# Optimization experiments

Hardware: AMD Instinct MI355X
Metric: run time of the kernel (lower is better)

Reference implementation:

```python
import jax, jax.numpy as jnp
import numpy as np

B, X, Y, Z = 8, 32, 32, 32
Dx = Dy = Dz = 128
K = 256   # h_dim * k, k=1
H = 2     # h_out
EPS = 1e-5


def _wn(V, g):
    # weight_norm with dim=None: W = g * V / ||V||_F (g scalar)
    return (g / jnp.linalg.norm(V)) * V


def setup_inputs() -> dict:
    key = jax.random.key(0)
    ks = jax.random.split(key, 8)
    x = jax.random.normal(ks[0], (B, X, Dx), jnp.float32)
    y = jax.random.normal(ks[1], (B, Y, Dy), jnp.float32)
    z = jax.random.normal(ks[2], (B, Z, Dz), jnp.float32)
    Vx = jax.random.normal(ks[3], (K, Dx), jnp.float32) * 0.05
    Vy = jax.random.normal(ks[4], (K, Dy), jnp.float32) * 0.05
    Vz = jax.random.normal(ks[5], (K, Dz), jnp.float32) * 0.05
    Vh = jax.random.normal(ks[6], (H, K), jnp.float32) * 0.05
    return {
        "x": x, "y": y, "z": z,
        "Vx": Vx, "gx": jnp.linalg.norm(Vx), "bx": jnp.zeros((K,), jnp.float32),
        "Vy": Vy, "gy": jnp.linalg.norm(Vy), "by": jnp.zeros((K,), jnp.float32),
        "Vz": Vz, "gz": jnp.linalg.norm(Vz), "bz": jnp.zeros((K,), jnp.float32),
        "Vh": Vh, "gh": jnp.linalg.norm(Vh), "bh": jnp.zeros((H,), jnp.float32),
        "gamma": jnp.ones((K,), jnp.float32), "beta": jnp.zeros((K,), jnp.float32),
    }


def reference(x, y, z, Vx, gx, bx, Vy, gy, by, Vz, gz, bz, Vh, gh, bh, gamma, beta):
    relu = jax.nn.relu
    _x = relu(x @ _wn(Vx, gx).T + bx)  # [B,X,K]
    _y = relu(y @ _wn(Vy, gy).T + by)  # [B,Y,K]
    _z = relu(z @ _wn(Vz, gz).T + bz)  # [B,Z,K]
    # trilinear outer product: [B,X,Y,Z,K] (memory-explosive intermediate)
    xyz = jnp.einsum('bxk,byk,bzk->bxyzk', _x, _y, _z)
    att = jnp.einsum('bxyzk,hk->bhxyz', xyz, _wn(Vh, gh)) + bh[None, :, None, None, None]
    # softmax over flattened X*Y*Z per head
    att = jax.nn.softmax(att.reshape(B, H, -1), axis=-1).reshape(B, H, X, Y, Z)
    # attention pooling, summed over all h_out heads (equals the torch loop)
    att_sum = att.sum(axis=1)  # [B,X,Y,Z]
    logits = jnp.einsum('bxk,byk,bzk,bxyz->bk', _x, _y, _z, att_sum)  # [B,K]
    # BatchNorm1d (training-mode batch stats, biased variance)
    mean = logits.mean(axis=0)
    var = logits.var(axis=0)
    out = (logits - mean) / jnp.sqrt(var + EPS) * gamma + beta
    return (out, att)
```

## Files before the change

### kernel.cpp

```cpp
#include <hip/hip_runtime.h>
#include <math.h>

#define BB 8
#define XD 32
#define DD 128
#define KK 256
#define HH 2
#define XYZ 32768
#define EPSV 1e-5f

#define WS_X    0
#define WS_Y    65536
#define WS_Z    131072
#define WS_RAW  196608
#define WS_SM   (WS_RAW + 524288)
#define WS_LOG  (WS_SM + 1024)

__global__ void __launch_bounds__(256)
tan_proj_kernel(const float* x, const float* y, const float* z,
                const float* Vx, const float* Vy, const float* Vz,
                const float* gx, const float* gy, const float* gz,
                const float* bx, const float* by, const float* bz,
                float* ws) {
    __shared__ float lin[4 * DD];
    __shared__ float wred[4];
    int bid = blockIdx.x;
    int which = bid >> 6;
    int rgrp = bid & 63;
    int r0 = rgrp * 4;
    const float *in, *V, *g, *bias;
    float* outp;
    if (which == 0)      { in = x; V = Vx; g = gx; bias = bx; outp = ws + WS_X; }
    else if (which == 1) { in = y; V = Vy; g = gy; bias = by; outp = ws + WS_Y; }
    else                 { in = z; V = Vz; g = gz; bias = bz; outp = ws + WS_Z; }
    int t = threadIdx.x;
    {
        int f0 = t, f1 = t + 256;
        lin[f0] = in[(r0 + (f0 >> 7)) * DD + (f0 & 127)];
        lin[f1] = in[(r0 + (f1 >> 7)) * DD + (f1 & 127)];
    }
    __syncthreads();
    const float4* v4 = (const float4*)(V + t * DD);
    const float4* l4 = (const float4*)lin;
    float a0 = 0.f, a1 = 0.f, a2 = 0.f, a3 = 0.f, ssp = 0.f;
#pragma unroll 8
    for (int d4 = 0; d4 < DD / 4; ++d4) {
        float4 a = v4[d4];
        ssp += a.x * a.x + a.y * a.y + a.z * a.z + a.w * a.w;
        float4 b0 = l4[d4];
        float4 b1 = l4[32 + d4];
        float4 b2 = l4[64 + d4];
        float4 b3 = l4[96 + d4];
        a0 += a.x * b0.x + a.y * b0.y + a.z * b0.z + a.w * b0.w;
        a1 += a.x * b1.x + a.y * b1.y + a.z * b1.z + a.w * b1.w;
        a2 += a.x * b2.x + a.y * b2.y + a.z * b2.z + a.w * b2.w;
        a3 += a.x * b3.x + a.y * b3.y + a.z * b3.z + a.w * b3.w;
    }
#pragma unroll
    for (int o = 32; o > 0; o >>= 1) ssp += __shfl_xor(ssp, o);
    if ((t & 63) == 0) wred[t >> 6] = ssp;
    __syncthreads();
    float ss = wred[0] + wred[1] + wred[2] + wred[3];
    float scale = g[0] * rsqrtf(ss);
    float bv = bias[t];
    outp[(r0 + 0) * KK + t] = fmaxf(a0 * scale + bv, 0.f);
    outp[(r0 + 1) * KK + t] = fmaxf(a1 * scale + bv, 0.f);
    outp[(r0 + 2) * KK + t] = fmaxf(a2 * scale + bv, 0.f);
    outp[(r0 + 3) * KK + t] = fmaxf(a3 * scale + bv, 0.f);
}

__global__ void __launch_bounds__(256)
tan_score_kernel(const float* Vh, const float* gh, const float* bh, float* ws) {
    __shared__ float ys[32 * 256];
    __shared__ float zs[32 * 256];
    __shared__ float shh;
    __shared__ float smred[4][4];
    int t = threadIdx.x;
    int bb = blockIdx.x >> 5;
    int xx = blockIdx.x & 31;
    const float* _xb = ws + WS_X + (bb * 32 + xx) * KK;
    const float* _yb = ws + WS_Y + bb * 8192;
    const float* _zb = ws + WS_Z + bb * 8192;

    if (t < 64) {
        float4 h1 = *(const float4*)(Vh + t * 8);
        float4 h2 = *(const float4*)(Vh + t * 8 + 4);
        float hs = h1.x * h1.x + h1.y * h1.y + h1.z * h1.z + h1.w * h1.w
                 + h2.x * h2.x + h2.y * h2.y + h2.z * h2.z + h2.w * h2.w;
#pragma unroll
        for (int o = 32; o > 0; o >>= 1) hs += __shfl_xor(hs, o);
        if (t == 0) shh = hs;
    }

#pragma unroll
    for (int i = 0; i < 8; ++i) {
        int flat = i * 1024 + t * 4;
        int row = flat >> 8;
        int k = flat & 255;
        int gsw = (((k >> 2) ^ (row & 7)) << 2);
        *(float4*)(ys + row * 256 + gsw) = *(const float4*)(_yb + flat);
        *(float4*)(zs + row * 256 + gsw) = *(const float4*)(_zb + flat);
    }
    __syncthreads();
    float sh = gh[0] * rsqrtf(shh);

    int ty = t >> 4;
    int tz = t & 15;
    int y0 = ty, y1 = ty + 16;
    int z0 = tz, z1 = tz + 15 + 1;
    int ysw0 = (y0 & 7), ysw1 = (y1 & 7);
    int zsw0 = (z0 & 7), zsw1 = (z1 & 7);

    float a000 = 0.f, a001 = 0.f, a010 = 0.f, a011 = 0.f;
    float a100 = 0.f, a101 = 0.f, a110 = 0.f, a111 = 0.f;

#pragma unroll 4
    for (int kc = 0; kc < 256; kc += 4) {
        int g = kc >> 2;
        float4 xv  = *(const float4*)(_xb + kc);
        float4 vh0 = *(const float4*)(Vh + kc);
        float4 vh1 = *(const float4*)(Vh + KK + kc);
        float4 ya = *(const float4*)(ys + y0 * 256 + ((g ^ ysw0) << 2));
        float4 yb = *(const float4*)(ys + y1 * 256 + ((g ^ ysw1) << 2));
        float4 za = *(const float4*)(zs + z0 * 256 + ((g ^ zsw0) << 2));
        float4 zb = *(const float4*)(zs + z1 * 256 + ((g ^ zsw1) << 2));
#define TAN_STEP(c) { \
        float xs = sh * xv.c; \
        float w0 = xs * vh0.c, w1 = xs * vh1.c; \
        float t00 = w0 * ya.c, t01 = w0 * yb.c; \
        float t10 = w1 * ya.c, t11 = w1 * yb.c; \
        a000 = fmaf(t00, za.c, a000); a001 = fmaf(t00, zb.c, a001); \
        a010 = fmaf(t01, za.c, a010); a011 = fmaf(t01, zb.c, a011); \
        a100 = fmaf(t10, za.c, a100); a101 = fmaf(t10, zb.c, a101); \
        a110 = fmaf(t11, za.c, a110); a111 = fmaf(t11, zb.c, a111); }
        TAN_STEP(x) TAN_STEP(y) TAN_STEP(z) TAN_STEP(w)
#undef TAN_STEP
    }

    float b0 = bh[0], b1 = bh[1];
    a000 += b0; a001 += b0; a010 += b0; a011 += b0;
    a100 += b1; a101 += b1; a110 += b1; a111 += b1;
    float* r0 = ws + WS_RAW + (bb * 2 + 0) * XYZ + xx * 1024;
    float* r1 = r0 + XYZ;
    r0[y0 * 32 + z0] = a000;  r0[y0 * 32 + z1] = a001;
    r0[y1 * 32 + z0] = a010;  r0[y1 * 32 + z1] = a011;
    r1[y0 * 32 + z0] = a100;  r1[y0 * 32 + z1] = a101;
    r1[y1 * 32 + z0] = a110;  r1[y1 * 32 + z1] = a111;

    float m0 = fmaxf(fmaxf(a000, a001), fmaxf(a010, a011));
    float l0 = __expf(a000 - m0) + __expf(a001 - m0)
             + __expf(a010 - m0) + __expf(a011 - m0);
    float m1 = fmaxf(fmaxf(a100, a101), fmaxf(a110, a111));
    float l1 = __expf(a100 - m1) + __expf(a101 - m1)
             + __expf(a110 - m1) + __expf(a111 - m1);
#pragma unroll
    for (int o = 1; o < 64; o <<= 1) {
        float mo = __shfl_xor(m0, o), lo = __shfl_xor(l0, o);
        float nm = fmaxf(m0, mo);
        l0 = l0 * __expf(m0 - nm) + lo * __expf(mo - nm); m0 = nm;
        mo = __shfl_xor(m1, o); lo = __shfl_xor(l1, o);
        nm = fmaxf(m1, mo);
        l1 = l1 * __expf(m1 - nm) + lo * __expf(mo - nm); m1 = nm;
    }
    if ((t & 63) == 0) {
        int w = t >> 6;
        smred[w][0] = m0; smred[w][1] = l0;
        smred[w][2] = m1; smred[w][3] = l1;
    }
    __syncthreads();
    if (t == 0) {
        float M0 = smred[0][0], L0 = smred[0][1];
        float M1 = smred[0][2], L1 = smred[0][3];
#pragma unroll
        for (int w = 1; w < 4; ++w) {
            float nm = fmaxf(M0, smred[w][0]);
            L0 = L0 * __expf(M0 - nm) + smred[w][1] * __expf(smred[w][0] - nm);
            M0 = nm;
            nm = fmaxf(M1, smred[w][2]);
            L1 = L1 * __expf(M1 - nm) + smred[w][3] * __expf(smred[w][2] - nm);
            M1 = nm;
        }
        float* sm = ws + WS_SM + (bb * 32 + xx) * 4;
        sm[0] = M0; sm[1] = L0; sm[2] = M1; sm[3] = L1;
    }
}

__global__ void __launch_bounds__(256)
tan_logits_kernel(float* ws, float* out) {
    __shared__ float as4[1024];
    __shared__ float cons[4];
    int b = blockIdx.x >> 5;
    int x = blockIdx.x & 31;
    int t = threadIdx.x;
    const float* _zb = ws + WS_Z + b * 8192;
    float zreg[32];
#pragma unroll
    for (int zi = 0; zi < 32; ++zi) zreg[zi] = _zb[zi * 256 + t];

    if (t < 64) {
        const float* sm = ws + WS_SM + (b * 32 + (t & 31)) * 4;
        float4 p = *(const float4*)sm;
        float m0 = p.x, l0 = p.y, m1 = p.z, l1 = p.w;
#pragma unroll
        for (int o = 1; o < 32; o <<= 1) {
            float mo = __shfl_xor(m0, o), lo = __shfl_xor(l0, o);
            float nm = fmaxf(m0, mo);
            l0 = l0 * __expf(m0 - nm) + lo * __expf(mo - nm); m0 = nm;
            mo = __shfl_xor(m1, o); lo = __shfl_xor(l1, o);
            nm = fmaxf(m1, mo);
            l1 = l1 * __expf(m1 - nm) + lo * __expf(mo - nm); m1 = nm;
        }
        if (t == 0) {
            cons[0] = m0; cons[1] = 1.f / l0;
            cons[2] = m1; cons[3] = 1.f / l1;
        }
    }
    __syncthreads();
    float M0 = cons[0], inv0 = cons[1], M1 = cons[2], inv1 = cons[3];
    const float* r0 = ws + WS_RAW + (b * 2) * XYZ + x * 1024;
    const float* r1 = r0 + XYZ;
    float* o0 = out + BB * KK + (b * 2) * XYZ + x * 1024;
    float* o1 = o0 + XYZ;
#pragma unroll
    for (int i = t; i < 1024; i += 256) {
        float a0 = __expf(r0[i] - M0) * inv0;
        float a1 = __expf(r1[i] - M1) * inv1;
        o0[i] = a0; o1[i] = a1;
        as4[i] = a0 + a1;
    }
    __syncthreads();

    const float* _yb = ws + WS_Y + b * 8192;
    float acc = 0.f;
#pragma unroll 4
    for (int y = 0; y < 32; ++y) {
        float s = 0.f;
        const float4* ar = (const float4*)(as4 + y * 32);
#pragma unroll
        for (int j = 0; j < 8; ++j) {
            float4 a = ar[j];
            s += a.x * zreg[j * 4] + a.y * zreg[j * 4 + 1]
               + a.z * zreg[j * 4 + 2] + a.w * zreg[j * 4 + 3];
        }
        acc = fmaf(_yb[y * 256 + t], s, acc);
    }
    float xv = ws[WS_X + (b * 32 + x) * 256 + t];
    atomicAdd(ws + WS_LOG + b * 256 + t, xv * acc);
}

__global__ void __launch_bounds__(256)
tan_bn_kernel(const float* ws, const float* gamma, const float* beta, float* out) {
    int k = threadIdx.x;
    const float* lgp = ws + WS_LOG;
    float lg[BB];
#pragma unroll
    for (int b = 0; b < BB; ++b) lg[b] = lgp[b * 256 + k];
    float mean = 0.f;
#pragma unroll
    for (int b = 0; b < BB; ++b) mean += lg[b];
    mean *= 0.125f;
    float var = 0.f;
#pragma unroll
    for (int b = 0; b < BB; ++b) { float d = lg[b] - mean; var += d * d; }
    var *= 0.125f;
    float inv = rsqrtf(var + EPSV);
    float gm = gamma[k], bt = beta[k];
#pragma unroll
    for (int b = 0; b < BB; ++b)
        out[b * 256 + k] = (lg[b] - mean) * inv * gm + bt;
}

extern "C" void kernel_launch(void* const* d_in, const int* in_sizes, int n_in,
                              void* d_out, int out_size, void* d_ws, size_t ws_size,
                              hipStream_t stream) {
    (void)in_sizes; (void)n_in; (void)out_size; (void)ws_size;
    const float* x     = (const float*)d_in[0];
    const float* y     = (const float*)d_in[1];
    const float* z     = (const float*)d_in[2];
    const float* Vx    = (const float*)d_in[3];
    const float* gx    = (const float*)d_in[4];
    const float* bx    = (const float*)d_in[5];
    const float* Vy    = (const float*)d_in[6];
    const float* gy    = (const float*)d_in[7];
    const float* by    = (const float*)d_in[8];
    const float* Vz    = (const float*)d_in[9];
    const float* gz    = (const float*)d_in[10];
    const float* bz    = (const float*)d_in[11];
    const float* Vh    = (const float*)d_in[12];
    const float* gh    = (const float*)d_in[13];
    const float* bh    = (const float*)d_in[14];
    const float* gamma = (const float*)d_in[15];
    const float* beta  = (const float*)d_in[16];
    float* ws  = (float*)d_ws;
    float* out = (float*)d_out;

    hipMemsetAsync(ws + WS_LOG, 0, 2048 * sizeof(float), stream);
    tan_proj_kernel<<<192, 256, 0, stream>>>(x, y, z, Vx, Vy, Vz,
                                             gx, gy, gz, bx, by, bz, ws);
    tan_score_kernel<<<256, 256, 0, stream>>>(Vh, gh, bh, ws);
    tan_logits_kernel<<<256, 256, 0, stream>>>(ws, out);
    tan_bn_kernel<<<1, 256, 0, stream>>>(ws, gamma, beta, out);
}
```

Measured before the change: 121.7 us.

## Fuse all stages into one cooperative kernel with grid syncs, keep scores on-chip

Replaces the memset and four kernel launches with a single cooperative kernel that separates projection, scoring, softmax/pooling and batchnorm with grid-wide syncs. The raw attention scores stay in registers across the softmax-statistics sync, so the 2 MB workspace round trip is gone. Y/Z values are read from shared memory instead of global, and attention output is written with coalesced float4 stores. The trade-off is grid.sync cost and a requirement that all 256 blocks be co-resident; the 64 KB of shared memory per block may limit occupancy.

```diff
diff --git a/kernel.cpp b/kernel.cpp
--- a/kernel.cpp
+++ b/kernel.cpp
@@ -1,96 +1,103 @@
 #include <hip/hip_runtime.h>
+#include <hip/hip_cooperative_groups.h>
 #include <math.h>
 
+namespace cg = cooperative_groups;
+
 #define BB 8
-#define XD 32
 #define DD 128
 #define KK 256
-#define HH 2
 #define XYZ 32768
 #define EPSV 1e-5f
 
 #define WS_X    0
 #define WS_Y    65536
 #define WS_Z    131072
-#define WS_RAW  196608
-#define WS_SM   (WS_RAW + 524288)
-#define WS_LOG  (WS_SM + 1024)
+#define WS_SM   196608
+#define WS_SHH  (WS_SM + 1024)
+#define WS_LOG  (WS_SHH + 16)
 
 __global__ void __launch_bounds__(256)
-tan_proj_kernel(const float* x, const float* y, const float* z,
-                const float* Vx, const float* Vy, const float* Vz,
-                const float* gx, const float* gy, const float* gz,
-                const float* bx, const float* by, const float* bz,
-                float* ws) {
+tan_fused_kernel(const float* x, const float* y, const float* z,
+                 const float* Vx, const float* Vy, const float* Vz,
+                 const float* gx, const float* gy, const float* gz,
+                 const float* bx, const float* by, const float* bz,
+                 const float* Vh, const float* gh, const float* bh,
+                 const float* gamma, const float* beta,
+                 float* ws, float* out) {
+    cg::grid_group grid = cg::this_grid();
+    __shared__ float smem[16384];
     __shared__ float lin[4 * DD];
     __shared__ float wred[4];
+    __shared__ float smred[4][4];
+    __shared__ float cons[4];
+
+    int t = threadIdx.x;
     int bid = blockIdx.x;
-    int which = bid >> 6;
-    int rgrp = bid & 63;
-    int r0 = rgrp * 4;
-    const float *in, *V, *g, *bias;
-    float* outp;
-    if (which == 0)      { in = x; V = Vx; g = gx; bias = bx; outp = ws + WS_X; }
-    else if (which == 1) { in = y; V = Vy; g = gy; bias = by; outp = ws + WS_Y; }
-    else                 { in = z; V = Vz; g = gz; bias = bz; outp = ws + WS_Z; }
-    int t = threadIdx.x;
-    {
+
+    if (bid < 192) {
+        int which = bid >> 6;
+        int r0 = (bid & 63) * 4;
+        const float *in, *V, *g, *bias;
+        float* outp;
+        if (which == 0)      { in = x; V = Vx; g = gx; bias = bx; outp = ws + WS_X; }
+        else if (which == 1) { in = y; V = Vy; g = gy; bias = by; outp = ws + WS_Y; }
+        else                 { in = z; V = Vz; g = gz; bias = bz; outp = ws + WS_Z; }
         int f0 = t, f1 = t + 256;
         lin[f0] = in[(r0 + (f0 >> 7)) * DD + (f0 & 127)];
         lin[f1] = in[(r0 + (f1 >> 7)) * DD + (f1 & 127)];
-    }
-    __syncthreads();
-    const float4* v4 = (const float4*)(V + t * DD);
-    const float4* l4 = (const float4*)lin;
-    float a0 = 0.f, a1 = 0.f, a2 = 0.f, a3 = 0.f, ssp = 0.f;
+        __syncthreads();
+        const float4* v4 = (const float4*)(V + t * DD);
+        const float4* l4 = (const float4*)lin;
+        float a0 = 0.f, a1 = 0.f, a2 = 0.f, a3 = 0.f, ssp = 0.f;
 #pragma unroll 8
-    for (int d4 = 0; d4 < DD / 4; ++d4) {
-        float4 a = v4[d4];
-        ssp += a.x * a.x + a.y * a.y + a.z * a.z + a.w * a.w;
-        float4 b0 = l4[d4];
-        float4 b1 = l4[32 + d4];
-        float4 b2 = l4[64 + d4];
-        float4 b3 = l4[96 + d4];
-        a0 += a.x * b0.x + a.y * b0.y + a.z * b0.z + a.w * b0.w;
-        a1 += a.x * b1.x + a.y * b1.y + a.z * b1.z + a.w * b1.w;
-        a2 += a.x * b2.x + a.y * b2.y + a.z * b2.z + a.w * b2.w;
-        a3 += a.x * b3.x + a.y * b3.y + a.z * b3.z + a.w * b3.w;
-    }
-#pragma unroll
-    for (int o = 32; o > 0; o >>= 1) ssp += __shfl_xor(ssp, o);
-    if ((t & 63) == 0) wred[t >> 6] = ssp;
-    __syncthreads();
-    float ss = wred[0] + wred[1] + wred[2] + wred[3];
-    float scale = g[0] * rsqrtf(ss);
-    float bv = bias[t];
-    outp[(r0 + 0) * KK + t] = fmaxf(a0 * scale + bv, 0.f);
-    outp[(r0 + 1) * KK + t] = fmaxf(a1 * scale + bv, 0.f);
-    outp[(r0 + 2) * KK + t] = fmaxf(a2 * scale + bv, 0.f);
-    outp[(r0 + 3) * KK + t] = fmaxf(a3 * scale + bv, 0.f);
-}
-
-__global__ void __launch_bounds__(256)
-tan_score_kernel(const float* Vh, const float* gh, const float* bh, float* ws) {
-    __shared__ float ys[32 * 256];
-    __shared__ float zs[32 * 256];
-    __shared__ float shh;
-    __shared__ float smred[4][4];
-    int t = threadIdx.x;
-    int bb = blockIdx.x >> 5;
-    int xx = blockIdx.x & 31;
+        for (int d4 = 0; d4 < DD / 4; ++d4) {
+            float4 a = v4[d4];
+            ssp += a.x * a.x + a.y * a.y + a.z * a.z + a.w * a.w;
+            float4 b0 = l4[d4];
+            float4 b1 = l4[32 + d4];
+            float4 b2 = l4[64 + d4];
+            float4 b3 = l4[96 + d4];
+            a0 += a.x * b0.x + a.y * b0.y + a.z * b0.z + a.w * b0.w;
+            a1 += a.x * b1.x + a.y * b1.y + a.z * b1.z + a.w * b1.w;
+            a2 += a.x * b2.x + a.y * b2.y + a.z * b2.z + a.w * b2.w;
+            a3 += a.x * b3.x + a.y * b3.y + a.z * b3.z + a.w * b3.w;
+        }
+#pragma unroll
+        for (int o = 32; o > 0; o >>= 1) ssp += __shfl_xor(ssp, o);
+        if ((t & 63) == 0) wred[t >> 6] = ssp;
+        __syncthreads();
+        float ss = wred[0] + wred[1] + wred[2] + wred[3];
+        float scale = g[0] * rsqrtf(ss);
+        float bv = bias[t];
+        outp[(r0 + 0) * KK + t] = fmaxf(a0 * scale + bv, 0.f);
+        outp[(r0 + 1) * KK + t] = fmaxf(a1 * scale + bv, 0.f);
+        outp[(r0 + 2) * KK + t] = fmaxf(a2 * scale + bv, 0.f);
+        outp[(r0 + 3) * KK + t] = fmaxf(a3 * scale + bv, 0.f);
+    } else if (bid == 192) {
+        for (int i = t; i < 2048; i += 256) ws[WS_LOG + i] = 0.f;
+    } else if (bid == 193) {
+        if (t < 64) {
+            float4 h1 = *(const float4*)(Vh + t * 8);
+            float4 h2 = *(const float4*)(Vh + t * 8 + 4);
+            float hs = h1.x * h1.x + h1.y * h1.y + h1.z * h1.z + h1.w * h1.w
+                     + h2.x * h2.x + h2.y * h2.y + h2.z * h2.z + h2.w * h2.w;
+#pragma unroll
+            for (int o = 32; o > 0; o >>= 1) hs += __shfl_xor(hs, o);
+            if (t == 0) ws[WS_SHH] = hs;
+        }
+    }
+    __threadfence();
+    grid.sync();
+
+    int bb = bid >> 5;
+    int xx = bid & 31;
     const float* _xb = ws + WS_X + (bb * 32 + xx) * KK;
     const float* _yb = ws + WS_Y + bb * 8192;
     const float* _zb = ws + WS_Z + bb * 8192;
-
-    if (t < 64) {
-        float4 h1 = *(const float4*)(Vh + t * 8);
-        float4 h2 = *(const float4*)(Vh + t * 8 + 4);
-        float hs = h1.x * h1.x + h1.y * h1.y + h1.z * h1.z + h1.w * h1.w
-                 + h2.x * h2.x + h2.y * h2.y + h2.z * h2.z + h2.w * h2.w;
-#pragma unroll
-        for (int o = 32; o > 0; o >>= 1) hs += __shfl_xor(hs, o);
-        if (t == 0) shh = hs;
-    }
+    float sh = gh[0] * rsqrtf(ws[WS_SHH]);
+    float* ys = smem;
+    float* zs = smem + 8192;
 
 #pragma unroll
     for (int i = 0; i < 8; ++i) {
@@ -102,12 +109,11 @@
         *(float4*)(zs + row * 256 + gsw) = *(const float4*)(_zb + flat);
     }
     __syncthreads();
-    float sh = gh[0] * rsqrtf(shh);
 
     int ty = t >> 4;
     int tz = t & 15;
     int y0 = ty, y1 = ty + 16;
-    int z0 = tz, z1 = tz + 15 + 1;
+    int z0 = tz, z1 = tz + 16;
     int ysw0 = (y0 & 7), ysw1 = (y1 & 7);
     int zsw0 = (z0 & 7), zsw1 = (z1 & 7);
 
@@ -140,12 +146,14 @@
     float b0 = bh[0], b1 = bh[1];
     a000 += b0; a001 += b0; a010 += b0; a011 += b0;
     a100 += b1; a101 += b1; a110 += b1; a111 += b1;
-    float* r0 = ws + WS_RAW + (bb * 2 + 0) * XYZ + xx * 1024;
-    float* r1 = r0 + XYZ;
-    r0[y0 * 32 + z0] = a000;  r0[y0 * 32 + z1] = a001;
-    r0[y1 * 32 + z0] = a010;  r0[y1 * 32 + z1] = a011;
-    r1[y0 * 32 + z0] = a100;  r1[y0 * 32 + z1] = a101;
-    r1[y1 * 32 + z0] = a110;  r1[y1 * 32 + z1] = a111;
+
+    float yreg[32], zreg[32];
+#pragma unroll
+    for (int r = 0; r < 32; ++r) {
+        int sw = ((((t >> 2) ^ (r & 7)) << 2) | (t & 3));
+        yreg[r] = ys[r * 256 + sw];
+        zreg[r] = zs[r * 256 + sw];
+    }
 
     float m0 = fmaxf(fmaxf(a000, a001), fmaxf(a010, a011));
     float l0 = __expf(a000 - m0) + __expf(a001 - m0)
@@ -183,91 +191,92 @@
         float* sm = ws + WS_SM + (bb * 32 + xx) * 4;
         sm[0] = M0; sm[1] = L0; sm[2] = M1; sm[3] = L1;
     }
-}
-
-__global__ void __launch_bounds__(256)
-tan_logits_kernel(float* ws, float* out) {
-    __shared__ float as4[1024];
-    __shared__ float cons[4];
-    int b = blockIdx.x >> 5;
-    int x = blockIdx.x & 31;
-    int t = threadIdx.x;
-    const float* _zb = ws + WS_Z + b * 8192;
-    float zreg[32];
-#pragma unroll
-    for (int zi = 0; zi < 32; ++zi) zreg[zi] = _zb[zi * 256 + t];
+    __threadfence();
+    grid.sync();
 
     if (t < 64) {
-        const float* sm = ws + WS_SM + (b * 32 + (t & 31)) * 4;
+        const float* sm = ws + WS_SM + (bb * 32 + (t & 31)) * 4;
         float4 p = *(const float4*)sm;
-        float m0 = p.x, l0 = p.y, m1 = p.z, l1 = p.w;
+        float fm0 = p.x, fl0 = p.y, fm1 = p.z, fl1 = p.w;
 #pragma unroll
         for (int o = 1; o < 32; o <<= 1) {
-            float mo = __shfl_xor(m0, o), lo = __shfl_xor(l0, o);
-            float nm = fmaxf(m0, mo);
-            l0 = l0 * __expf(m0 - nm) + lo * __expf(mo - nm); m0 = nm;
-            mo = __shfl_xor(m1, o); lo = __shfl_xor(l1, o);
-            nm = fmaxf(m1, mo);
-            l1 = l1 * __expf(m1 - nm) + lo * __expf(mo - nm); m1 = nm;
+            float mo = __shfl_xor(fm0, o), lo = __shfl_xor(fl0, o);
+            float nm = fmaxf(fm0, mo);
+            fl0 = fl0 * __expf(fm0 - nm) + lo * __expf(mo - nm); fm0 = nm;
+            mo = __shfl_xor(fm1, o); lo = __shfl_xor(fl1, o);
+            nm = fmaxf(fm1, mo);
+            fl1 = fl1 * __expf(fm1 - nm) + lo * __expf(mo - nm); fm1 = nm;
         }
         if (t == 0) {
-            cons[0] = m0; cons[1] = 1.f / l0;
-            cons[2] = m1; cons[3] = 1.f / l1;
+            cons[0] = fm0; cons[1] = 1.f / fl0;
+            cons[2] = fm1; cons[3] = 1.f / fl1;
         }
     }
     __syncthreads();
     float M0 = cons[0], inv0 = cons[1], M1 = cons[2], inv1 = cons[3];
-    const float* r0 = ws + WS_RAW + (b * 2) * XYZ + x * 1024;
-    const float* r1 = r0 + XYZ;
-    float* o0 = out + BB * KK + (b * 2) * XYZ + x * 1024;
-    float* o1 = o0 + XYZ;
-#pragma unroll
-    for (int i = t; i < 1024; i += 256) {
-        float a0 = __expf(r0[i] - M0) * inv0;
-        float a1 = __expf(r1[i] - M1) * inv1;
-        o0[i] = a0; o1[i] = a1;
-        as4[i] = a0 + a1;
-    }
+
+    float* e0p = smem;
+    float* e1p = smem + 1024;
+    float* as4 = smem + 2048;
+    float e000 = __expf(a000 - M0) * inv0;
+    float e001 = __expf(a001 - M0) * inv0;
+    float e010 = __expf(a010 - M0) * inv0;
+    float e011 = __expf(a011 - M0) * inv0;
+    float e100 = __expf(a100 - M1) * inv1;
+    float e101 = __expf(a101 - M1) * inv1;
+    float e110 = __expf(a110 - M1) * inv1;
+    float e111 = __expf(a111 - M1) * inv1;
+    e0p[y0 * 32 + z0] = e000;  e0p[y0 * 32 + z1] = e001;
+    e0p[y1 * 32 + z0] = e010;  e0p[y1 * 32 + z1] = e011;
+    e1p[y0 * 32 + z0] = e100;  e1p[y0 * 32 + z1] = e101;
+    e1p[y1 * 32 + z0] = e110;  e1p[y1 * 32 + z1] = e111;
+    as4[y0 * 32 + z0] = e000 + e100;  as4[y0 * 32 + z1] = e001 + e101;
+    as4[y1 * 32 + z0] = e010 + e110;  as4[y1 * 32 + z1] = e011 + e111;
     __syncthreads();
 
-    const float* _yb = ws + WS_Y + b * 8192;
+    float4* o0 = (float4*)(out + BB * KK + (bb * 2) * XYZ + xx * 1024);
+    float4* o1 = o0 + XYZ / 4;
+    o0[t] = ((const float4*)e0p)[t];
+    o1[t] = ((const float4*)e1p)[t];
+
     float acc = 0.f;
 #pragma unroll 4
-    for (int y = 0; y < 32; ++y) {
+    for (int yy = 0; yy < 32; ++yy) {
         float s = 0.f;
-        const float4* ar = (const float4*)(as4 + y * 32);
+        const float4* ar = (const float4*)(as4 + yy * 32);
 #pragma unroll
         for (int j = 0; j < 8; ++j) {
             float4 a = ar[j];
             s += a.x * zreg[j * 4] + a.y * zreg[j * 4 + 1]
                + a.z * zreg[j * 4 + 2] + a.w * zreg[j * 4 + 3];
         }
-        acc = fmaf(_yb[y * 256 + t], s, acc);
-    }
-    float xv = ws[WS_X + (b * 32 + x) * 256 + t];
-    atomicAdd(ws + WS_LOG + b * 256 + t, xv * acc);
-}
-
-__global__ void __launch_bounds__(256)
-tan_bn_kernel(const float* ws, const float* gamma, const float* beta, float* out) {
-    int k = threadIdx.x;
-    const float* lgp = ws + WS_LOG;
-    float lg[BB];
-#pragma unroll
-    for (int b = 0; b < BB; ++b) lg[b] = lgp[b * 256 + k];
-    float mean = 0.f;
-#pragma unroll
-    for (int b = 0; b < BB; ++b) mean += lg[b];
-    mean *= 0.125f;
-    float var = 0.f;
-#pragma unroll
-    for (int b = 0; b < BB; ++b) { float d = lg[b] - mean; var += d * d; }
-    var *= 0.125f;
-    float inv = rsqrtf(var + EPSV);
-    float gm = gamma[k], bt = beta[k];
-#pragma unroll
-    for (int b = 0; b < BB; ++b)
-        out[b * 256 + k] = (lg[b] - mean) * inv * gm + bt;
+        acc = fmaf(yreg[yy], s, acc);
+    }
+    float xv = ws[WS_X + (bb * 32 + xx) * 256 + t];
+    atomicAdd(ws + WS_LOG + bb * 256 + t, xv * acc);
+    __threadfence();
+    grid.sync();
+
+    if (bid == 0) {
+        int k = t;
+        const float* lgp = ws + WS_LOG;
+        float lg[BB];
+#pragma unroll
+        for (int b = 0; b < BB; ++b) lg[b] = lgp[b * 256 + k];
+        float mean = 0.f;
+#pragma unroll
+        for (int b = 0; b < BB; ++b) mean += lg[b];
+        mean *= 0.125f;
+        float var = 0.f;
+#pragma unroll
+        for (int b = 0; b < BB; ++b) { float d = lg[b] - mean; var += d * d; }
+        var *= 0.125f;
+        float inv = rsqrtf(var + EPSV);
+        float gm = gamma[k], bt = beta[k];
+#pragma unroll
+        for (int b = 0; b < BB; ++b)
+            out[b * 256 + k] = (lg[b] - mean) * inv * gm + bt;
+    }
 }
 
 extern "C" void kernel_launch(void* const* d_in, const int* in_sizes, int n_in,
@@ -294,10 +303,15 @@
     float* ws  = (float*)d_ws;
     float* out = (float*)d_out;
 
-    hipMemsetAsync(ws + WS_LOG, 0, 2048 * sizeof(float), stream);
-    tan_proj_kernel<<<192, 256, 0, stream>>>(x, y, z, Vx, Vy, Vz,
-                                             gx, gy, gz, bx, by, bz, ws);
-    tan_score_kernel<<<256, 256, 0, stream>>>(Vh, gh, bh, ws);
-    tan_logits_kernel<<<256, 256, 0, stream>>>(ws, out);
-    tan_bn_kernel<<<1, 256, 0, stream>>>(ws, gamma, beta, out);
+    void* args[] = {
+        (void*)&x, (void*)&y, (void*)&z,
+        (void*)&Vx, (void*)&Vy, (void*)&Vz,
+        (void*)&gx, (void*)&gy, (void*)&gz,
+        (void*)&bx, (void*)&by, (void*)&bz,
+        (void*)&Vh, (void*)&gh, (void*)&bh,
+        (void*)&gamma, (void*)&beta,
+        (void*)&ws, (void*)&out,
+    };
+    hipLaunchCooperativeKernel((void*)tan_fused_kernel, dim3(256), dim3(256),
+                               args, 0, stream);
 }
```

New measurement: 288.2 us. +136.8%, slower.
